# Kernel optimization log

Measured on AMD Instinct MI355X. Metric: run time of the kernel, lower is better.

The kernel has to match this reference:

```python
import jax, jax.numpy as jnp
import numpy as np

B, N, E, D = 32, 4096, 8192, 128


def setup_inputs() -> dict:
    key = jax.random.key(0)
    ks = jax.random.split(key, 6)
    atom_state = jax.random.normal(ks[0], (B, N, D), dtype=jnp.float32)
    messages = jax.random.normal(ks[1], (B, E, D), dtype=jnp.float32)
    connectivity = jax.random.randint(ks[2], (B, E, 2), 0, N, dtype=jnp.int32)
    kernel = jax.random.normal(ks[3], (D, 3 * D), dtype=jnp.float32) * 0.05
    recurrent_kernel = jax.random.normal(ks[4], (D, 3 * D), dtype=jnp.float32) * 0.05
    bias = jnp.zeros((2, 3 * D), dtype=jnp.float32)
    return {"atom_state": atom_state, "messages": messages,
            "connectivity": connectivity, "kernel": kernel,
            "recurrent_kernel": recurrent_kernel, "bias": bias}


def reference(atom_state, messages, connectivity, kernel, recurrent_kernel, bias):
    b, n, d = atom_state.shape
    # --- Reduce: scatter-add messages onto target atoms ---
    tgt_idx = connectivity[:, :, 1]                       # [B,E]
    offset = (jnp.arange(b, dtype=tgt_idx.dtype) * n)[:, None]
    flat_idx = (tgt_idx + offset).reshape(-1)             # [B*E]
    flat_msgs = messages.reshape(-1, d)                   # [B*E,D]
    aggregated = jax.ops.segment_sum(flat_msgs, flat_idx, num_segments=b * n)  # [B*N,D]
    # --- GRUCell (Keras default: reset_after=True, sigmoid/tanh) ---
    h = atom_state.reshape(-1, d)                         # [B*N,D]
    matrix_x = aggregated @ kernel + bias[0]              # [B*N,3D]
    matrix_h = h @ recurrent_kernel + bias[1]             # [B*N,3D]
    x_z, x_r, x_h = jnp.split(matrix_x, 3, axis=-1)
    r_z, r_r, r_h = jnp.split(matrix_h, 3, axis=-1)
    z = jax.nn.sigmoid(x_z + r_z)
    r = jax.nn.sigmoid(x_r + r_r)
    hh = jnp.tanh(x_h + r * r_h)
    h_new = z * h + (1.0 - z) * hh
    return h_new.reshape(b, n, d)
```

## Files before the change

kernel.cpp:

```cpp
#include <hip/hip_runtime.h>
#include <hip/hip_bf16.h>
#include <stdint.h>

#define BB 32
#define NN 4096
#define EE 8192
#define DD 128
#define MM (BB * NN)
#define THREE_D (3 * DD)
#define CAP 32
#define PF 8

typedef __bf16 bf16x8 __attribute__((ext_vector_type(8)));
typedef __bf16 bf16x2 __attribute__((ext_vector_type(2)));
typedef float  f32x4  __attribute__((ext_vector_type(4)));
typedef float  f32x2  __attribute__((ext_vector_type(2)));

#define AGG_BYTES ((size_t)MM * DD * 2)
#define WT_OFF    AGG_BYTES
#define WT_BYTES  ((size_t)2 * THREE_D * DD * 2)
#define CNT_OFF   (WT_OFF + WT_BYTES)
#define CNT_BYTES ((size_t)MM * 4)
#define BKT_OFF   (CNT_OFF + CNT_BYTES)

__global__ void transpose_weights(const float* __restrict__ w0,
                                  const float* __restrict__ w1,
                                  __bf16* __restrict__ wt,
                                  int* __restrict__ counts) {
    int tid = blockIdx.x * blockDim.x + threadIdx.x;
    for (int i = tid; i < MM; i += 2 * THREE_D * DD)
        counts[i] = 0;
    int mat = tid / (THREE_D * DD);
    int rem = tid % (THREE_D * DD);
    int col = rem / DD;
    int k   = rem % DD;
    const float* src = mat ? w1 : w0;
    wt[tid] = (__bf16)src[k * THREE_D + col];
}

__global__ void scatter_ids(const int* __restrict__ conn,
                            int* __restrict__ counts,
                            int* __restrict__ bucket) {
    int e = blockIdx.x * 256 + threadIdx.x;
    int b = e >> 13;
    int2 pr = ((const int2*)conn)[e];
    int node = b * NN + pr.y;
    int pos = atomicAdd(&counts[node], 1);
    if (pos < CAP) bucket[node * CAP + pos] = e;
}

#define TPB_GEMM 8
#define AGP 136
#define HP  132
__launch_bounds__(512, 2)
__global__ void gru_gemm_fused(const float* __restrict__ messages,
                               const int* __restrict__ counts,
                               const int* __restrict__ bucket,
                               const float* __restrict__ h_in,
                               const __bf16* __restrict__ wt,
                               const float* __restrict__ bias,
                               float* __restrict__ out) {
    const int tid  = threadIdx.x;
    const int wave = tid >> 6;
    const int lane = tid & 63;
    const int quad = lane >> 4;
    const int l16  = lane & 15;

    __shared__ __bf16 aT[2][16 * AGP];
    __shared__ float  hT[2][16 * HP];

    bf16x8 bfrag[3][2][4];
    for (int p = 0; p < 3; ++p)
        for (int m = 0; m < 2; ++m)
            for (int ko = 0; ko < 4; ++ko)
                bfrag[p][m][ko] = *(const bf16x8*)(wt
                    + ((size_t)(m * THREE_D + p * 128 + wave * 16 + l16)) * DD
                    + ko * 32 + quad * 8);

    const int j = wave * 16 + l16;
    const float b0z = bias[j];
    const float b0r = bias[DD + j];
    const float b0h = bias[2 * DD + j];
    const float b1z = bias[THREE_D + j];
    const float b1r = bias[THREE_D + DD + j];
    const float b1h = bias[THREE_D + 2 * DD + j];

    const int tile0 = blockIdx.x * TPB_GEMM;

    f32x4 sh;
    auto load_h = [&](int tb) {
        sh = *(const f32x4*)(h_in + (size_t)tb * 2048 + tid * 4);
    };
    auto write_h = [&](int bf) {
        *(f32x4*)&hT[bf][(tid >> 5) * HP + (tid & 31) * 4] = sh;
    };

    const int ar = tid >> 4;
    const int ac = (tid & 15) * 8;
    int cnt = 0;
    int ids[PF];
    f32x4 ma[4], mb[4];
    auto agg_issue = [&](int tb) {
        if (tid < 256) {
            int node = tb * 16 + ar;
            cnt = counts[node];
            if (cnt > CAP) cnt = CAP;
            *(int4*)&ids[0] = *(const int4*)(bucket + (size_t)node * CAP);
            *(int4*)&ids[4] = *(const int4*)(bucket + (size_t)node * CAP + 4);
            for (int i = 0; i < 4; ++i) {
                int e = (i < cnt) ? ids[i] : 0;
                ma[i] = *(const f32x4*)(messages + (size_t)e * DD + ac);
                mb[i] = *(const f32x4*)(messages + (size_t)e * DD + ac + 4);
            }
        }
    };
    auto agg_finish = [&](int tb, int bf) {
        if (tid < 256) {
            f32x4 s0 = (f32x4){0.f, 0.f, 0.f, 0.f};
            f32x4 s1 = (f32x4){0.f, 0.f, 0.f, 0.f};
            for (int i = 0; i < 4; ++i)
                if (i < cnt) { s0 += ma[i]; s1 += mb[i]; }
            if (cnt > 4) {
                for (int i = 4; i < 8; ++i) {
                    int e = (i < cnt) ? ids[i] : 0;
                    f32x4 va = *(const f32x4*)(messages + (size_t)e * DD + ac);
                    f32x4 vb = *(const f32x4*)(messages + (size_t)e * DD + ac + 4);
                    if (i < cnt) { s0 += va; s1 += vb; }
                }
                for (int i = PF; i < cnt; ++i) {
                    int e = bucket[(size_t)(tb * 16 + ar) * CAP + i];
                    s0 += *(const f32x4*)(messages + (size_t)e * DD + ac);
                    s1 += *(const f32x4*)(messages + (size_t)e * DD + ac + 4);
                }
            }
            bf16x8 o;
            for (int q = 0; q < 4; ++q) {
                o[q]     = (__bf16)s0[q];
                o[q + 4] = (__bf16)s1[q];
            }
            *(bf16x8*)&aT[bf][ar * AGP + ac] = o;
        }
    };

    agg_issue(tile0);
    load_h(tile0);
    agg_finish(tile0, 0);
    write_h(0);

    int buf = 0;
    for (int t = 0; t < TPB_GEMM; ++t) {
        __syncthreads();
        const int tb = tile0 + t;
        if (t + 1 < TPB_GEMM) {
            agg_issue(tb + 1);
            load_h(tb + 1);
        }

        f32x4 acc[3][2];
        for (int p = 0; p < 3; ++p)
            for (int m = 0; m < 2; ++m)
                acc[p][m] = (f32x4){0.f, 0.f, 0.f, 0.f};

        for (int ko = 0; ko < 4; ++ko) {
            bf16x8 af = *(const bf16x8*)&aT[buf][l16 * AGP + ko * 32 + quad * 8];
            f32x4 h0 = *(const f32x4*)&hT[buf][l16 * HP + ko * 32 + quad * 8];
            f32x4 h1 = *(const f32x4*)&hT[buf][l16 * HP + ko * 32 + quad * 8 + 4];
            bf16x8 hg;
            for (int i = 0; i < 4; ++i) {
                hg[i]     = (__bf16)h0[i];
                hg[i + 4] = (__bf16)h1[i];
            }
            for (int p = 0; p < 3; ++p) {
                acc[p][0] = __builtin_amdgcn_mfma_f32_16x16x32_bf16(
                    af, bfrag[p][0][ko], acc[p][0], 0, 0, 0);
                acc[p][1] = __builtin_amdgcn_mfma_f32_16x16x32_bf16(
                    hg, bfrag[p][1][ko], acc[p][1], 0, 0, 0);
            }
        }

        if (t + 1 < TPB_GEMM) agg_finish(tb + 1, buf ^ 1);

        for (int rr = 0; rr < 4; ++rr) {
            int rl  = quad * 4 + rr;
            int row = tb * 16 + rl;
            float xz  = acc[0][0][rr] + b0z;
            float rz  = acc[0][1][rr] + b1z;
            float xr  = acc[1][0][rr] + b0r;
            float rrg = acc[1][1][rr] + b1r;
            float xh  = acc[2][0][rr] + b0h;
            float rh  = acc[2][1][rr] + b1h;
            float z   = 1.f / (1.f + __expf(-(xz + rz)));
            float rg  = 1.f / (1.f + __expf(-(xr + rrg)));
            float pre = xh + rg * rh;
            float hh  = 2.f / (1.f + __expf(-2.f * pre)) - 1.f;
            float hold = hT[buf][rl * HP + j];
            float o = z * hold + (1.f - z) * hh;
            out[(size_t)row * DD + j] = o;
        }

        if (t + 1 < TPB_GEMM) write_h(buf ^ 1);
        buf ^= 1;
    }
}

extern "C" void kernel_launch(void* const* d_in, const int* in_sizes, int n_in,
                              void* d_out, int out_size, void* d_ws, size_t ws_size,
                              hipStream_t stream) {
    const float* atom_state = (const float*)d_in[0];
    const float* messages   = (const float*)d_in[1];
    const int*   conn       = (const int*)d_in[2];
    const float* w0         = (const float*)d_in[3];
    const float* w1         = (const float*)d_in[4];
    const float* bias       = (const float*)d_in[5];
    float* out = (float*)d_out;

    __bf16* wt     = (__bf16*)((char*)d_ws + WT_OFF);
    int*    counts = (int*)((char*)d_ws + CNT_OFF);
    int*    bucket = (int*)((char*)d_ws + BKT_OFF);

    transpose_weights<<<(2 * THREE_D * DD) / 256, 256, 0, stream>>>(w0, w1, wt, counts);
    scatter_ids<<<(BB * EE) / 256, 256, 0, stream>>>(conn, counts, bucket);
    gru_gemm_fused<<<MM / (16 * TPB_GEMM), 512, 0, stream>>>(
        messages, counts, bucket, atom_state, wt, bias, out);
}
```

Before: 345.9 us.

## Replace atomic bucket scatter with per-batch shared-memory CSR build

Swaps the global-atomic bucket scheme (counts memset plus per-edge global atomics into fixed-capacity buckets) for one block per batch that builds a CSR in shared memory via histogram, prefix scan and placement. This also merges the weight transpose into the same launch, cutting one kernel launch. The GEMM kernel preloads offsets, counts and the first eight edge ids for its 128 rows into LDS, so the later message gathers read ids from LDS. It also drops the 32-per-node capacity cap. The risk is that only 32 blocks do the CSR build, which serialises that work onto a few CUs.

```diff
diff --git a/kernel.cpp b/kernel.cpp
--- a/kernel.cpp
+++ b/kernel.cpp
@@ -8,45 +8,74 @@
 #define DD 128
 #define MM (BB * NN)
 #define THREE_D (3 * DD)
-#define CAP 32
-#define PF 8
 
 typedef __bf16 bf16x8 __attribute__((ext_vector_type(8)));
-typedef __bf16 bf16x2 __attribute__((ext_vector_type(2)));
 typedef float  f32x4  __attribute__((ext_vector_type(4)));
-typedef float  f32x2  __attribute__((ext_vector_type(2)));
-
-#define AGG_BYTES ((size_t)MM * DD * 2)
-#define WT_OFF    AGG_BYTES
-#define WT_BYTES  ((size_t)2 * THREE_D * DD * 2)
-#define CNT_OFF   (WT_OFF + WT_BYTES)
-#define CNT_BYTES ((size_t)MM * 4)
-#define BKT_OFF   (CNT_OFF + CNT_BYTES)
-
-__global__ void transpose_weights(const float* __restrict__ w0,
-                                  const float* __restrict__ w1,
-                                  __bf16* __restrict__ wt,
-                                  int* __restrict__ counts) {
-    int tid = blockIdx.x * blockDim.x + threadIdx.x;
-    for (int i = tid; i < MM; i += 2 * THREE_D * DD)
-        counts[i] = 0;
-    int mat = tid / (THREE_D * DD);
-    int rem = tid % (THREE_D * DD);
-    int col = rem / DD;
-    int k   = rem % DD;
-    const float* src = mat ? w1 : w0;
-    wt[tid] = (__bf16)src[k * THREE_D + col];
-}
-
-__global__ void scatter_ids(const int* __restrict__ conn,
-                            int* __restrict__ counts,
-                            int* __restrict__ bucket) {
-    int e = blockIdx.x * 256 + threadIdx.x;
-    int b = e >> 13;
-    int2 pr = ((const int2*)conn)[e];
-    int node = b * NN + pr.y;
-    int pos = atomicAdd(&counts[node], 1);
-    if (pos < CAP) bucket[node * CAP + pos] = e;
+
+#define WT_OFF   0
+#define OFFC_OFF ((size_t)1 << 20)
+#define CSR_OFF  ((size_t)2 << 20)
+
+__global__ __launch_bounds__(256)
+void build_tables(const float* __restrict__ w0,
+                  const float* __restrict__ w1,
+                  const int* __restrict__ conn,
+                  __bf16* __restrict__ wt,
+                  int2* __restrict__ offcnt,
+                  int* __restrict__ csr) {
+    if (blockIdx.x >= BB) {
+        int tid = (blockIdx.x - BB) * 256 + threadIdx.x;
+        int mat = tid / (THREE_D * DD);
+        int rem = tid % (THREE_D * DD);
+        int col = rem / DD;
+        int k   = rem % DD;
+        const float* src = mat ? w1 : w0;
+        wt[tid] = (__bf16)src[k * THREE_D + col];
+        return;
+    }
+    __shared__ int tgtL[EE];
+    __shared__ int hist[NN];
+    __shared__ int part[256];
+    const int b   = blockIdx.x;
+    const int tid = threadIdx.x;
+    const int2* c2 = (const int2*)conn + (size_t)b * EE;
+
+    for (int k = 0; k < EE / 256; ++k) {
+        int e = k * 256 + tid;
+        tgtL[e] = c2[e].y;
+    }
+    for (int n = tid; n < NN; n += 256) hist[n] = 0;
+    __syncthreads();
+    for (int k = 0; k < EE / 256; ++k)
+        atomicAdd(&hist[tgtL[k * 256 + tid]], 1);
+    __syncthreads();
+
+    const int c0 = tid * 16;
+    int s = 0;
+    for (int i = 0; i < 16; ++i) s += hist[c0 + i];
+    part[tid] = s;
+    __syncthreads();
+    for (int d = 1; d < 256; d <<= 1) {
+        int v = (tid >= d) ? part[tid - d] : 0;
+        __syncthreads();
+        part[tid] += v;
+        __syncthreads();
+    }
+    int run = part[tid] - s;
+    for (int i = 0; i < 16; ++i) {
+        int c = hist[c0 + i];
+        offcnt[(size_t)b * NN + c0 + i] = (int2){b * EE + run, c};
+        hist[c0 + i] = run;
+        run += c;
+    }
+    __syncthreads();
+
+    for (int k = 0; k < EE / 256; ++k) {
+        int e = k * 256 + tid;
+        int t = tgtL[e];
+        int pos = atomicAdd(&hist[t], 1);
+        csr[(size_t)b * EE + pos] = b * EE + e;
+    }
 }
 
 #define TPB_GEMM 8
@@ -54,8 +83,8 @@
 #define HP  132
 __launch_bounds__(512, 2)
 __global__ void gru_gemm_fused(const float* __restrict__ messages,
-                               const int* __restrict__ counts,
-                               const int* __restrict__ bucket,
+                               const int2* __restrict__ offcnt,
+                               const int* __restrict__ csr,
                                const float* __restrict__ h_in,
                                const __bf16* __restrict__ wt,
                                const float* __restrict__ bias,
@@ -68,6 +97,9 @@
 
     __shared__ __bf16 aT[2][16 * AGP];
     __shared__ float  hT[2][16 * HP];
+    __shared__ int    idsL[128][8];
+    __shared__ int    cntL[128];
+    __shared__ int    baseL[128];
 
     bf16x8 bfrag[3][2][4];
     for (int p = 0; p < 3; ++p)
@@ -87,6 +119,15 @@
 
     const int tile0 = blockIdx.x * TPB_GEMM;
 
+    if (tid < 128) {
+        int2 oc = offcnt[(size_t)blockIdx.x * 128 + tid];
+        baseL[tid] = oc.x;
+        cntL[tid]  = oc.y;
+        #pragma unroll
+        for (int i = 0; i < 8; ++i)
+            idsL[tid][i] = csr[(size_t)oc.x + i];
+    }
+
     f32x4 sh;
     auto load_h = [&](int tb) {
         sh = *(const f32x4*)(h_in + (size_t)tb * 2048 + tid * 4);
@@ -98,42 +139,52 @@
     const int ar = tid >> 4;
     const int ac = (tid & 15) * 8;
     int cnt = 0;
-    int ids[PF];
+    int ids2[4];
     f32x4 ma[4], mb[4];
-    auto agg_issue = [&](int tb) {
+    auto msg_issue = [&](int rb) {
         if (tid < 256) {
-            int node = tb * 16 + ar;
-            cnt = counts[node];
-            if (cnt > CAP) cnt = CAP;
-            *(int4*)&ids[0] = *(const int4*)(bucket + (size_t)node * CAP);
-            *(int4*)&ids[4] = *(const int4*)(bucket + (size_t)node * CAP + 4);
-            for (int i = 0; i < 4; ++i) {
-                int e = (i < cnt) ? ids[i] : 0;
-                ma[i] = *(const f32x4*)(messages + (size_t)e * DD + ac);
-                mb[i] = *(const f32x4*)(messages + (size_t)e * DD + ac + 4);
-            }
-        }
-    };
-    auto agg_finish = [&](int tb, int bf) {
+            cnt = cntL[rb];
+            int i0 = idsL[rb][0], i1 = idsL[rb][1];
+            int i2 = idsL[rb][2], i3 = idsL[rb][3];
+            ids2[0] = idsL[rb][4]; ids2[1] = idsL[rb][5];
+            ids2[2] = idsL[rb][6]; ids2[3] = idsL[rb][7];
+            int e0 = (0 < cnt) ? i0 : 0;
+            int e1 = (1 < cnt) ? i1 : 0;
+            int e2 = (2 < cnt) ? i2 : 0;
+            int e3 = (3 < cnt) ? i3 : 0;
+            ma[0] = *(const f32x4*)(messages + (size_t)e0 * DD + ac);
+            mb[0] = *(const f32x4*)(messages + (size_t)e0 * DD + ac + 4);
+            ma[1] = *(const f32x4*)(messages + (size_t)e1 * DD + ac);
+            mb[1] = *(const f32x4*)(messages + (size_t)e1 * DD + ac + 4);
+            ma[2] = *(const f32x4*)(messages + (size_t)e2 * DD + ac);
+            mb[2] = *(const f32x4*)(messages + (size_t)e2 * DD + ac + 4);
+            ma[3] = *(const f32x4*)(messages + (size_t)e3 * DD + ac);
+            mb[3] = *(const f32x4*)(messages + (size_t)e3 * DD + ac + 4);
+        }
+    };
+    auto agg_finish = [&](int rb, int bf) {
         if (tid < 256) {
             f32x4 s0 = (f32x4){0.f, 0.f, 0.f, 0.f};
             f32x4 s1 = (f32x4){0.f, 0.f, 0.f, 0.f};
+            #pragma unroll
             for (int i = 0; i < 4; ++i)
                 if (i < cnt) { s0 += ma[i]; s1 += mb[i]; }
             if (cnt > 4) {
+                #pragma unroll
                 for (int i = 4; i < 8; ++i) {
-                    int e = (i < cnt) ? ids[i] : 0;
+                    int e = (i < cnt) ? ids2[i - 4] : 0;
                     f32x4 va = *(const f32x4*)(messages + (size_t)e * DD + ac);
                     f32x4 vb = *(const f32x4*)(messages + (size_t)e * DD + ac + 4);
                     if (i < cnt) { s0 += va; s1 += vb; }
                 }
-                for (int i = PF; i < cnt; ++i) {
-                    int e = bucket[(size_t)(tb * 16 + ar) * CAP + i];
+                for (int i = 8; i < cnt; ++i) {
+                    int e = csr[(size_t)baseL[rb] + i];
                     s0 += *(const f32x4*)(messages + (size_t)e * DD + ac);
                     s1 += *(const f32x4*)(messages + (size_t)e * DD + ac + 4);
                 }
             }
             bf16x8 o;
+            #pragma unroll
             for (int q = 0; q < 4; ++q) {
                 o[q]     = (__bf16)s0[q];
                 o[q + 4] = (__bf16)s1[q];
@@ -142,9 +193,10 @@
         }
     };
 
-    agg_issue(tile0);
+    __syncthreads();
+    msg_issue(ar);
     load_h(tile0);
-    agg_finish(tile0, 0);
+    agg_finish(ar, 0);
     write_h(0);
 
     int buf = 0;
@@ -152,7 +204,7 @@
         __syncthreads();
         const int tb = tile0 + t;
         if (t + 1 < TPB_GEMM) {
-            agg_issue(tb + 1);
+            msg_issue((t + 1) * 16 + ar);
             load_h(tb + 1);
         }
 
@@ -178,7 +230,7 @@
             }
         }
 
-        if (t + 1 < TPB_GEMM) agg_finish(tb + 1, buf ^ 1);
+        if (t + 1 < TPB_GEMM) agg_finish((t + 1) * 16 + ar, buf ^ 1);
 
         for (int rr = 0; rr < 4; ++rr) {
             int rl  = quad * 4 + rr;
@@ -215,11 +267,11 @@
     float* out = (float*)d_out;
 
     __bf16* wt     = (__bf16*)((char*)d_ws + WT_OFF);
-    int*    counts = (int*)((char*)d_ws + CNT_OFF);
-    int*    bucket = (int*)((char*)d_ws + BKT_OFF);
-
-    transpose_weights<<<(2 * THREE_D * DD) / 256, 256, 0, stream>>>(w0, w1, wt, counts);
-    scatter_ids<<<(BB * EE) / 256, 256, 0, stream>>>(conn, counts, bucket);
+    int2*   offcnt = (int2*)((char*)d_ws + OFFC_OFF);
+    int*    csr    = (int*)((char*)d_ws + CSR_OFF);
+
+    build_tables<<<BB + (2 * THREE_D * DD) / 256, 256, 0, stream>>>(
+        w0, w1, conn, wt, offcnt, csr);
     gru_gemm_fused<<<MM / (16 * TPB_GEMM), 512, 0, stream>>>(
-        messages, counts, bucket, atom_state, wt, bias, out);
+        messages, offcnt, csr, atom_state, wt, bias, out);
 }
```

New measurement: 318.7 us. 7.9% less time.
